# Kernel optimization log

Hardware: AMD Instinct MI355X
Metric: run time of the kernel (lower is better)

The kernel has to match this reference:

```python
import jax, jax.numpy as jnp
import numpy as np

T, B, H = 64, 2048, 256
H1, H2, OUT = 64, 64, 601


def setup_inputs() -> dict:
    key = jax.random.key(0)
    ks = jax.random.split(key, 12)
    s = 1.0 / np.sqrt(H)
    inp = {
        "x": jax.random.normal(ks[0], (T, B, 1), jnp.float32),
        "h0": jax.random.normal(ks[1], (1, B, H), jnp.float32),
        # PyTorch GRU params: gate order (r, z, n)
        "w_ih": jax.random.uniform(ks[2], (3 * H, 1), jnp.float32, -s, s),
        "w_hh": jax.random.uniform(ks[3], (3 * H, H), jnp.float32, -s, s),
        "b_ih": jax.random.uniform(ks[4], (3 * H,), jnp.float32, -s, s),
        "b_hh": jax.random.uniform(ks[5], (3 * H,), jnp.float32, -s, s),
        "w1": jax.random.normal(ks[6], (H, H1), jnp.float32) / np.sqrt(H),
        "b1": jnp.zeros((H1,), jnp.float32),
        "w2": jax.random.normal(ks[7], (H1, H2), jnp.float32) / np.sqrt(H1),
        "b2": jnp.zeros((H2,), jnp.float32),
        "w3": jax.random.normal(ks[8], (H2, OUT), jnp.float32) / np.sqrt(H2),
        "b3": jnp.zeros((OUT,), jnp.float32),
    }
    return inp


def _gru_scan(x, h0, w_ih, w_hh, b_ih, b_hh):
    # x: [T,B,1], h0: [B,H]. PyTorch GRU cell, gate order (r, z, n).
    def step(h, x_t):
        gi = x_t @ w_ih.T + b_ih          # [B,3H]
        gh = h @ w_hh.T + b_hh            # [B,3H]
        i_r, i_z, i_n = jnp.split(gi, 3, axis=-1)
        h_r, h_z, h_n = jnp.split(gh, 3, axis=-1)
        r = jax.nn.sigmoid(i_r + h_r)
        z = jax.nn.sigmoid(i_z + h_z)
        n = jnp.tanh(i_n + r * h_n)
        h_new = (1.0 - z) * n + z * h
        return h_new, h_new
    h_last, ys = jax.lax.scan(step, h0, x)
    return ys, h_last


def reference(x, h0, w_ih, w_hh, b_ih, b_hh, w1, b1, w2, b2, w3, b3):
    ys, h_last = _gru_scan(x, h0[0], w_ih, w_hh, b_ih, b_hh)  # ys: [T,B,H]
    h = jax.nn.elu(ys @ w1 + b1)
    h = jax.nn.elu(h @ w2 + b2)
    y = h @ w3 + b3                       # [T,B,601]
    h1 = h_last[None]                     # [1,B,H]
    return (y, h1)
```

## Files before the change

### kernel.cpp

```cpp
#include <hip/hip_runtime.h>
#include <cstdint>
#include <cstddef>

typedef _Float16 f16;
typedef _Float16 f16x8 __attribute__((ext_vector_type(8)));
typedef float f32x4 __attribute__((ext_vector_type(4)));

#define LOG2E 1.4426950408889634f

__device__ __forceinline__ float fast_rcp(float x) { return __builtin_amdgcn_rcpf(x); }
__device__ __forceinline__ float sigmoid_f(float x) { return fast_rcp(1.f + exp2f(-LOG2E * x)); }
__device__ __forceinline__ float tanh_f(float x)    { return 1.f - 2.f * fast_rcp(1.f + exp2f(2.f * LOG2E * x)); }
__device__ __forceinline__ float elu_f(float x)     { return x > 0.f ? x : exp2f(LOG2E * x) - 1.f; }

__global__ void pack_weights(const float* __restrict__ w_hh, const float* __restrict__ w1,
                             const float* __restrict__ w2, const float* __restrict__ w3,
                             f16* __restrict__ wpkh, f16* __restrict__ wpk1,
                             f16* __restrict__ wpk2, f16* __restrict__ wpk3) {
    int s = blockIdx.x * 256 + threadIdx.x;
    if (s < 24576) {
        int l = s & 63, kt = (s >> 6) & 7, jt = s >> 9;
        int j = jt * 16 + (l & 15), k = kt * 32 + (l >> 4) * 8;
        const float* src = w_hh + (size_t)j * 256 + k;
        f16x8 v;
        #pragma unroll
        for (int e = 0; e < 8; ++e) v[e] = (f16)src[e];
        *(f16x8*)(wpkh + (size_t)s * 8) = v;
    } else if (s < 26624) {
        int q = s - 24576;
        int l = q & 63, jt = (q >> 6) & 3, kt = q >> 8;
        int j = jt * 16 + (l & 15), k = kt * 32 + (l >> 4) * 8;
        f16x8 v;
        #pragma unroll
        for (int e = 0; e < 8; ++e) v[e] = (f16)w1[(size_t)(k + e) * 64 + j];
        *(f16x8*)(wpk1 + (size_t)q * 8) = v;
    } else if (s < 27136) {
        int q = s - 26624;
        int l = q & 63, jt = (q >> 6) & 3, kt = q >> 8;
        int j = jt * 16 + (l & 15), k = kt * 32 + (l >> 4) * 8;
        f16x8 v;
        #pragma unroll
        for (int e = 0; e < 8; ++e) v[e] = (f16)w2[(size_t)(k + e) * 64 + j];
        *(f16x8*)(wpk2 + (size_t)q * 8) = v;
    } else if (s < 32000) {
        int q = s - 27136;
        int l = q & 63, rr = q >> 6;
        int jt = rr % 38, kt = rr / 38;
        int j = jt * 16 + (l & 15), k = kt * 32 + (l >> 4) * 8;
        f16x8 v;
        #pragma unroll
        for (int e = 0; e < 8; ++e) v[e] = (j < 601) ? (f16)w3[(size_t)(k + e) * 601 + j] : (f16)0.f;
        *(f16x8*)(wpk3 + (size_t)q * 8) = v;
    }
}

template <int ALIGNED>
__global__ __launch_bounds__(512, 2)
void gru_kernel(const float* __restrict__ x, const float* __restrict__ h0,
                const float* __restrict__ w_ih, const float* __restrict__ b_ih,
                const float* __restrict__ b_hh, const f16* __restrict__ wpkh,
                char* __restrict__ ys_base, float* __restrict__ h1_out) {
    __shared__ f16 h_lds[2][16][264];
    __shared__ float x_lds[64][16];

    const int tid = threadIdx.x, lane = tid & 63, wid = tid >> 6;
    const int l15 = lane & 15, lg = lane >> 4;
    const int b0 = blockIdx.x * 16;
    const long STRIDE = ALIGNED ? 512 : 2404;

    f16x8 wf[6][8];
    #pragma unroll
    for (int g = 0; g < 3; ++g)
        #pragma unroll
        for (int sub = 0; sub < 2; ++sub) {
            int jt = g * 16 + wid * 2 + sub;
            #pragma unroll
            for (int kt = 0; kt < 8; ++kt)
                wf[g * 2 + sub][kt] = *(const f16x8*)(wpkh + (((size_t)jt * 8 + kt) * 64 + lane) * 8);
        }

    float wi[3][2], bacc[3][2], bin[2];
    #pragma unroll
    for (int g = 0; g < 3; ++g)
        #pragma unroll
        for (int sub = 0; sub < 2; ++sub) {
            int j = g * 256 + wid * 32 + sub * 16 + l15;
            wi[g][sub] = w_ih[j];
            bacc[g][sub] = (g < 2) ? (b_ih[j] + b_hh[j]) : b_hh[j];
            if (g == 2) bin[sub] = b_ih[j];
        }

    float hp[2][4];
    #pragma unroll
    for (int sub = 0; sub < 2; ++sub)
        #pragma unroll
        for (int r = 0; r < 4; ++r)
            hp[sub][r] = h0[(size_t)(b0 + lg * 4 + r) * 256 + wid * 32 + sub * 16 + l15];

    {
        int row = tid >> 5, k0 = (tid & 31) * 8;
        const float* src = h0 + (size_t)(b0 + row) * 256 + k0;
        f16x8 v;
        #pragma unroll
        for (int e = 0; e < 8; ++e) v[e] = (f16)src[e];
        *(f16x8*)&h_lds[0][row][k0] = v;
        #pragma unroll
        for (int i = 0; i < 2; ++i) {
            int n = tid + i * 512, tt = n >> 4, bb = n & 15;
            x_lds[tt][bb] = x[(size_t)tt * 2048 + b0 + bb];
        }
    }
    __syncthreads();

    for (int t = 0; t < 64; ++t) {
        const int cur = t & 1, nxt = cur ^ 1;

        f32x4 acc[6];
        #pragma unroll
        for (int i = 0; i < 6; ++i) {
            float b = bacc[i >> 1][i & 1];
            acc[i] = (f32x4){b, b, b, b};
        }
        #pragma unroll
        for (int kt = 0; kt < 8; ++kt) {
            f16x8 a = *(const f16x8*)&h_lds[cur][l15][kt * 32 + lg * 8];
            #pragma unroll
            for (int i = 0; i < 6; ++i)
                acc[i] = __builtin_amdgcn_mfma_f32_16x16x32_f16(a, wf[i][kt], acc[i], 0, 0, 0);
        }

        f32x4 xv4 = *(const f32x4*)&x_lds[t][lg * 4];
        #pragma unroll
        for (int sub = 0; sub < 2; ++sub)
            #pragma unroll
            for (int r = 0; r < 4; ++r) {
                float xv = xv4[r];
                float rg = sigmoid_f(xv * wi[0][sub] + acc[0 + sub][r]);
                float zg = sigmoid_f(xv * wi[1][sub] + acc[2 + sub][r]);
                float ng = tanh_f(xv * wi[2][sub] + bin[sub] + rg * acc[4 + sub][r]);
                float hn = ng + zg * (hp[sub][r] - ng);
                hp[sub][r] = hn;
                h_lds[nxt][lg * 4 + r][wid * 32 + sub * 16 + l15] = (f16)hn;
            }
        __syncthreads();

        {
            int row = tid >> 5, k0 = (tid & 31) * 8;
            f16x8 v = *(const f16x8*)&h_lds[nxt][row][k0];
            char* dst = ys_base + (size_t)(t * 2048 + b0 + row) * STRIDE + (size_t)k0 * 2;
            if (ALIGNED) {
                *(f16x8*)dst = v;
            } else {
                const uint32_t* u = (const uint32_t*)&v;
                uint32_t* d = (uint32_t*)dst;
                d[0] = u[0]; d[1] = u[1]; d[2] = u[2]; d[3] = u[3];
            }
        }
    }

    #pragma unroll
    for (int sub = 0; sub < 2; ++sub)
        #pragma unroll
        for (int r = 0; r < 4; ++r)
            h1_out[(size_t)(b0 + lg * 4 + r) * 256 + wid * 32 + sub * 16 + l15] = hp[sub][r];
}

template <int ALIGNED>
__global__ __launch_bounds__(256, 4)
void mlp_kernel(const char* __restrict__ ys_base, const f16* __restrict__ wpk1,
                const f16* __restrict__ wpk2, const f16* __restrict__ wpk3,
                const float* __restrict__ b1, const float* __restrict__ b2,
                const float* __restrict__ b3, float* __restrict__ y_out) {
    __shared__ f16 abuf[4][16][72];
    const int tid = threadIdx.x, lane = tid & 63, wid = tid >> 6;
    const int l15 = lane & 15, lg = lane >> 4;
    const size_t row0 = (size_t)blockIdx.x * 64 + wid * 16;
    const long STRIDE = ALIGNED ? 512 : 2404;

    f32x4 acc1[4];
    #pragma unroll
    for (int jt = 0; jt < 4; ++jt) { float b = b1[jt * 16 + l15]; acc1[jt] = (f32x4){b, b, b, b}; }
    #pragma unroll
    for (int kt = 0; kt < 8; ++kt) {
        f16x8 a;
        const char* src = ys_base + (row0 + l15) * STRIDE + (size_t)(kt * 32 + lg * 8) * 2;
        if (ALIGNED) a = *(const f16x8*)src;
        else {
            uint32_t u[4]; const uint32_t* sp = (const uint32_t*)src;
            u[0] = sp[0]; u[1] = sp[1]; u[2] = sp[2]; u[3] = sp[3];
            a = *(const f16x8*)u;
        }
        #pragma unroll
        for (int jt = 0; jt < 4; ++jt) {
            f16x8 bf = *(const f16x8*)(wpk1 + ((size_t)(kt * 4 + jt) * 64 + lane) * 8);
            acc1[jt] = __builtin_amdgcn_mfma_f32_16x16x32_f16(a, bf, acc1[jt], 0, 0, 0);
        }
    }
    #pragma unroll
    for (int jt = 0; jt < 4; ++jt)
        #pragma unroll
        for (int r = 0; r < 4; ++r)
            abuf[wid][lg * 4 + r][jt * 16 + l15] = (f16)elu_f(acc1[jt][r]);

    f16x8 af[2];
    #pragma unroll
    for (int kt = 0; kt < 2; ++kt) af[kt] = *(const f16x8*)&abuf[wid][l15][kt * 32 + lg * 8];
    f32x4 acc2[4];
    #pragma unroll
    for (int jt = 0; jt < 4; ++jt) { float b = b2[jt * 16 + l15]; acc2[jt] = (f32x4){b, b, b, b}; }
    #pragma unroll
    for (int kt = 0; kt < 2; ++kt)
        #pragma unroll
        for (int jt = 0; jt < 4; ++jt) {
            f16x8 bf = *(const f16x8*)(wpk2 + ((size_t)(kt * 4 + jt) * 64 + lane) * 8);
            acc2[jt] = __builtin_amdgcn_mfma_f32_16x16x32_f16(af[kt], bf, acc2[jt], 0, 0, 0);
        }
    #pragma unroll
    for (int jt = 0; jt < 4; ++jt)
        #pragma unroll
        for (int r = 0; r < 4; ++r)
            abuf[wid][lg * 4 + r][jt * 16 + l15] = (f16)elu_f(acc2[jt][r]);

    #pragma unroll
    for (int kt = 0; kt < 2; ++kt) af[kt] = *(const f16x8*)&abuf[wid][l15][kt * 32 + lg * 8];
    for (int jt = 0; jt < 38; ++jt) {
        int j = jt * 16 + l15;
        float b = (j < 601) ? b3[j] : 0.f;
        f32x4 acc = (f32x4){b, b, b, b};
        f16x8 bf0 = *(const f16x8*)(wpk3 + ((size_t)(0 * 38 + jt) * 64 + lane) * 8);
        f16x8 bf1 = *(const f16x8*)(wpk3 + ((size_t)(1 * 38 + jt) * 64 + lane) * 8);
        acc = __builtin_amdgcn_mfma_f32_16x16x32_f16(af[0], bf0, acc, 0, 0, 0);
        acc = __builtin_amdgcn_mfma_f32_16x16x32_f16(af[1], bf1, acc, 0, 0, 0);
        if (j < 601) {
            #pragma unroll
            for (int r = 0; r < 4; ++r)
                y_out[(row0 + lg * 4 + r) * 601 + j] = acc[r];
        }
    }
}

extern "C" void kernel_launch(void* const* d_in, const int* in_sizes, int n_in,
                              void* d_out, int out_size, void* d_ws, size_t ws_size,
                              hipStream_t stream) {
    const float* x    = (const float*)d_in[0];
    const float* h0   = (const float*)d_in[1];
    const float* w_ih = (const float*)d_in[2];
    const float* w_hh = (const float*)d_in[3];
    const float* b_ih = (const float*)d_in[4];
    const float* b_hh = (const float*)d_in[5];
    const float* w1   = (const float*)d_in[6];
    const float* b1   = (const float*)d_in[7];
    const float* w2   = (const float*)d_in[8];
    const float* b2   = (const float*)d_in[9];
    const float* w3   = (const float*)d_in[10];
    const float* b3   = (const float*)d_in[11];

    float* y_out  = (float*)d_out;
    float* h1_out = y_out + (size_t)64 * 2048 * 601;

    f16* wpkh = (f16*)d_ws;
    f16* wpk1 = (f16*)((char*)d_ws + 393216);
    f16* wpk2 = (f16*)((char*)d_ws + 425984);
    f16* wpk3 = (f16*)((char*)d_ws + 434176);
    const size_t YS_OFF = 524288;
    const size_t YS_BYTES = (size_t)131072 * 512;
    const bool ws_ok = ws_size >= YS_OFF + YS_BYTES;

    pack_weights<<<125, 256, 0, stream>>>(w_hh, w1, w2, w3, wpkh, wpk1, wpk2, wpk3);

    if (ws_ok) {
        char* ys = (char*)d_ws + YS_OFF;
        gru_kernel<1><<<128, 512, 0, stream>>>(x, h0, w_ih, b_ih, b_hh, wpkh, ys, h1_out);
        mlp_kernel<1><<<2048, 256, 0, stream>>>(ys, wpk1, wpk2, wpk3, b1, b2, b3, y_out);
    } else {
        char* ys = (char*)d_out;
        gru_kernel<0><<<128, 512, 0, stream>>>(x, h0, w_ih, b_ih, b_hh, wpkh, ys, h1_out);
        mlp_kernel<0><<<2048, 256, 0, stream>>>(ys, wpk1, wpk2, wpk3, b1, b2, b3, y_out);
    }
}
```

Baseline: 661.0 us.

## Stage MLP output through LDS for coalesced stores; split GRU MFMA by sub-tile

The final MLP layer now writes each 16x128 output chunk into a per-wave LDS buffer, then stores it row by row so consecutive lanes write consecutive columns. The previous scattered 4-row stores with stride 601 floats are replaced by coalesced row writes. The extra LDS use lowers launch bounds to 3 blocks per CU. Separately, the GRU step computes gates per sub-tile in two passes of 3 accumulators instead of 6, which cuts register pressure but loads the A fragments twice.

```diff
diff --git a/kernel.cpp b/kernel.cpp
--- a/kernel.cpp
+++ b/kernel.cpp
@@ -114,34 +114,34 @@
 
     for (int t = 0; t < 64; ++t) {
         const int cur = t & 1, nxt = cur ^ 1;
-
-        f32x4 acc[6];
-        #pragma unroll
-        for (int i = 0; i < 6; ++i) {
-            float b = bacc[i >> 1][i & 1];
-            acc[i] = (f32x4){b, b, b, b};
-        }
-        #pragma unroll
-        for (int kt = 0; kt < 8; ++kt) {
-            f16x8 a = *(const f16x8*)&h_lds[cur][l15][kt * 32 + lg * 8];
-            #pragma unroll
-            for (int i = 0; i < 6; ++i)
-                acc[i] = __builtin_amdgcn_mfma_f32_16x16x32_f16(a, wf[i][kt], acc[i], 0, 0, 0);
-        }
-
         f32x4 xv4 = *(const f32x4*)&x_lds[t][lg * 4];
-        #pragma unroll
-        for (int sub = 0; sub < 2; ++sub)
+
+        #pragma unroll
+        for (int sub = 0; sub < 2; ++sub) {
+            f32x4 acc[3];
+            #pragma unroll
+            for (int g = 0; g < 3; ++g) {
+                float b = bacc[g][sub];
+                acc[g] = (f32x4){b, b, b, b};
+            }
+            #pragma unroll
+            for (int kt = 0; kt < 8; ++kt) {
+                f16x8 a = *(const f16x8*)&h_lds[cur][l15][kt * 32 + lg * 8];
+                #pragma unroll
+                for (int g = 0; g < 3; ++g)
+                    acc[g] = __builtin_amdgcn_mfma_f32_16x16x32_f16(a, wf[g * 2 + sub][kt], acc[g], 0, 0, 0);
+            }
             #pragma unroll
             for (int r = 0; r < 4; ++r) {
                 float xv = xv4[r];
-                float rg = sigmoid_f(xv * wi[0][sub] + acc[0 + sub][r]);
-                float zg = sigmoid_f(xv * wi[1][sub] + acc[2 + sub][r]);
-                float ng = tanh_f(xv * wi[2][sub] + bin[sub] + rg * acc[4 + sub][r]);
+                float rg = sigmoid_f(xv * wi[0][sub] + acc[0][r]);
+                float zg = sigmoid_f(xv * wi[1][sub] + acc[1][r]);
+                float ng = tanh_f(xv * wi[2][sub] + bin[sub] + rg * acc[2][r]);
                 float hn = ng + zg * (hp[sub][r] - ng);
                 hp[sub][r] = hn;
                 h_lds[nxt][lg * 4 + r][wid * 32 + sub * 16 + l15] = (f16)hn;
             }
+        }
         __syncthreads();
 
         {
@@ -166,12 +166,13 @@
 }
 
 template <int ALIGNED>
-__global__ __launch_bounds__(256, 4)
+__global__ __launch_bounds__(256, 3)
 void mlp_kernel(const char* __restrict__ ys_base, const f16* __restrict__ wpk1,
                 const f16* __restrict__ wpk2, const f16* __restrict__ wpk3,
                 const float* __restrict__ b1, const float* __restrict__ b2,
                 const float* __restrict__ b3, float* __restrict__ y_out) {
     __shared__ f16 abuf[4][16][72];
+    __shared__ float ybuf[4][16][132];
     const int tid = threadIdx.x, lane = tid & 63, wid = tid >> 6;
     const int l15 = lane & 15, lg = lane >> 4;
     const size_t row0 = (size_t)blockIdx.x * 64 + wid * 16;
@@ -223,18 +224,29 @@
 
     #pragma unroll
     for (int kt = 0; kt < 2; ++kt) af[kt] = *(const f16x8*)&abuf[wid][l15][kt * 32 + lg * 8];
-    for (int jt = 0; jt < 38; ++jt) {
-        int j = jt * 16 + l15;
-        float b = (j < 601) ? b3[j] : 0.f;
-        f32x4 acc = (f32x4){b, b, b, b};
-        f16x8 bf0 = *(const f16x8*)(wpk3 + ((size_t)(0 * 38 + jt) * 64 + lane) * 8);
-        f16x8 bf1 = *(const f16x8*)(wpk3 + ((size_t)(1 * 38 + jt) * 64 + lane) * 8);
-        acc = __builtin_amdgcn_mfma_f32_16x16x32_f16(af[0], bf0, acc, 0, 0, 0);
-        acc = __builtin_amdgcn_mfma_f32_16x16x32_f16(af[1], bf1, acc, 0, 0, 0);
-        if (j < 601) {
+    for (int jc = 0; jc < 5; ++jc) {
+        const int njt = (jc < 4) ? 8 : 6;
+        for (int jt2 = 0; jt2 < njt; ++jt2) {
+            int jt = jc * 8 + jt2;
+            int j = jt * 16 + l15;
+            float b = (j < 601) ? b3[j] : 0.f;
+            f32x4 acc = (f32x4){b, b, b, b};
+            f16x8 bf0 = *(const f16x8*)(wpk3 + ((size_t)(0 * 38 + jt) * 64 + lane) * 8);
+            f16x8 bf1 = *(const f16x8*)(wpk3 + ((size_t)(1 * 38 + jt) * 64 + lane) * 8);
+            acc = __builtin_amdgcn_mfma_f32_16x16x32_f16(af[0], bf0, acc, 0, 0, 0);
+            acc = __builtin_amdgcn_mfma_f32_16x16x32_f16(af[1], bf1, acc, 0, 0, 0);
             #pragma unroll
             for (int r = 0; r < 4; ++r)
-                y_out[(row0 + lg * 4 + r) * 601 + j] = acc[r];
+                ybuf[wid][lg * 4 + r][jt2 * 16 + l15] = acc[r];
+        }
+        const int ncol = (jc < 4) ? 128 : 89;
+        for (int r16 = 0; r16 < 16; ++r16) {
+            #pragma unroll
+            for (int it = 0; it < 2; ++it) {
+                int c = it * 64 + lane;
+                if (c < ncol)
+                    y_out[(row0 + r16) * 601 + jc * 128 + c] = ybuf[wid][r16][c];
+            }
         }
     }
 }
```

Result: faster. 641.9 us (-2.9%).
